# Kernel optimization log

Hardware: AMD Instinct MI355X
Metric: run time of the kernel (lower is better)

## Reference

```python
import jax, jax.numpy as jnp
import numpy as np

QMAX = 7.0      # symmetric int4 magnitude
GROUP = 64      # weight quant group size along input dim
RANK = 32       # SVD low-rank correction rank
EPS = 1e-8


def quantize_act(x):
    # per-token symmetric int4 fake-quant: scale = max|x| / 7 over feature dim
    s = jnp.maximum(jnp.max(jnp.abs(x), axis=-1, keepdims=True) / QMAX, EPS)
    q = jnp.clip(jnp.round(x / s), -8.0, 7.0)
    return q * s


def quantize_weight(w):
    # per-output-channel, per-group (GROUP along input dim) symmetric int4 fake-quant
    O, D = w.shape
    wg = w.reshape(O, D // GROUP, GROUP)
    s = jnp.maximum(jnp.max(jnp.abs(wg), axis=-1, keepdims=True) / QMAX, EPS)
    q = jnp.clip(jnp.round(wg / s), -8.0, 7.0)
    return (q * s).reshape(O, D)


def setup_inputs() -> dict:
    key = jax.random.key(0)
    k0, k1, k2, k3 = jax.random.split(key, 4)
    dim_in, dim_out2 = 3072, 24576
    x = jax.random.normal(k0, (1, 4096, dim_in), dtype=jnp.float32)
    w_res = jax.random.normal(k1, (dim_out2, dim_in), dtype=jnp.float32) * 0.02
    lora_down = jax.random.normal(k2, (RANK, dim_in), dtype=jnp.float32) * 0.02
    lora_up = jax.random.normal(k3, (dim_out2, RANK), dtype=jnp.float32) * 0.02
    return {"x": x, "w_res": w_res, "lora_down": lora_down, "lora_up": lora_up}


def reference(x, w_res, lora_down, lora_up):
    # SVDQW4A4Linear: quantized residual matmul + fp low-rank correction
    xq = quantize_act(x)                        # [B, S, D]
    wq = quantize_weight(w_res)                 # [O, D]
    out = jnp.einsum('bsd,od->bso', xq, wq)
    out = out + jnp.einsum('bsr,or->bso', jnp.einsum('bsd,rd->bsr', x, lora_down), lora_up)
    # GEGLU epilogue: chunk(2, dim=-1), x * gelu(gate)  (torch F.gelu = exact erf)
    h, gate = jnp.split(out, 2, axis=-1)
    return h * jax.nn.gelu(gate, approximate=False)
```

## Files before the change

### kernel.cpp

```cpp
#include <hip/hip_runtime.h>
#include <hip/hip_bf16.h>
#include <math.h>

typedef __bf16 bf16_t;
typedef __bf16 bf16x4 __attribute__((ext_vector_type(4)));
typedef __bf16 bf16x8 __attribute__((ext_vector_type(8)));
typedef float  f32x4  __attribute__((ext_vector_type(4)));

#define DIN   3072
#define NOUT  24576
#define HALF  12288
#define MTOK  4096
#define BM    128
#define BN    128
#define BK    64

#define GLD16(gp, lp) \
    __builtin_amdgcn_global_load_lds((const __attribute__((address_space(1))) void*)(gp), \
                                     (__attribute__((address_space(3))) void*)(lp), 16, 0, 0)

__global__ __launch_bounds__(256) void k_quant_x(const float* __restrict__ x,
                                                 bf16_t* __restrict__ xq) {
    int m = blockIdx.x;
    int t = threadIdx.x;
    const float4* row = reinterpret_cast<const float4*>(x + (size_t)m * DIN);
    float4 v[3];
    float vm = 0.f;
#pragma unroll
    for (int i = 0; i < 3; ++i) {
        v[i] = row[t + i * 256];
        vm = fmaxf(vm, fmaxf(fmaxf(fabsf(v[i].x), fabsf(v[i].y)),
                             fmaxf(fabsf(v[i].z), fabsf(v[i].w))));
    }
#pragma unroll
    for (int d = 1; d < 64; d <<= 1) vm = fmaxf(vm, __shfl_xor(vm, d));
    __shared__ float sm[4];
    if ((t & 63) == 0) sm[t >> 6] = vm;
    __syncthreads();
    vm = fmaxf(fmaxf(sm[0], sm[1]), fmaxf(sm[2], sm[3]));
    float s = fmaxf(vm * (1.f / 7.f), 1e-8f);
    float inv = 1.f / s;
    bf16x4* orow = reinterpret_cast<bf16x4*>(xq + (size_t)m * DIN);
#pragma unroll
    for (int i = 0; i < 3; ++i) {
        bf16x4 o;
        o[0] = (bf16_t)(fminf(fmaxf(rintf(v[i].x * inv), -8.f), 7.f) * s);
        o[1] = (bf16_t)(fminf(fmaxf(rintf(v[i].y * inv), -8.f), 7.f) * s);
        o[2] = (bf16_t)(fminf(fmaxf(rintf(v[i].z * inv), -8.f), 7.f) * s);
        o[3] = (bf16_t)(fminf(fmaxf(rintf(v[i].w * inv), -8.f), 7.f) * s);
        orow[t + i * 256] = o;
    }
}

__global__ __launch_bounds__(256) void k_quant_w(const float* __restrict__ w,
                                                 bf16_t* __restrict__ wq) {
    size_t idx = (size_t)blockIdx.x * 256 + threadIdx.x;
    float4 v = reinterpret_cast<const float4*>(w)[idx];
    float vm = fmaxf(fmaxf(fabsf(v.x), fabsf(v.y)), fmaxf(fabsf(v.z), fabsf(v.w)));
    vm = fmaxf(vm, __shfl_xor(vm, 1));
    vm = fmaxf(vm, __shfl_xor(vm, 2));
    vm = fmaxf(vm, __shfl_xor(vm, 4));
    vm = fmaxf(vm, __shfl_xor(vm, 8));
    float s = fmaxf(vm * (1.f / 7.f), 1e-8f);
    float inv = 1.f / s;
    bf16x4 o;
    o[0] = (bf16_t)(fminf(fmaxf(rintf(v.x * inv), -8.f), 7.f) * s);
    o[1] = (bf16_t)(fminf(fmaxf(rintf(v.y * inv), -8.f), 7.f) * s);
    o[2] = (bf16_t)(fminf(fmaxf(rintf(v.z * inv), -8.f), 7.f) * s);
    o[3] = (bf16_t)(fminf(fmaxf(rintf(v.w * inv), -8.f), 7.f) * s);
    reinterpret_cast<bf16x4*>(wq)[idx] = o;
}

__global__ __launch_bounds__(256) void k_lora_t(const float* __restrict__ x,
                                                const float* __restrict__ ld,
                                                bf16_t* __restrict__ T) {
    int r = threadIdx.x & 31;
    int m = blockIdx.x * 8 + (threadIdx.x >> 5);
    const float4* xr = reinterpret_cast<const float4*>(x + (size_t)m * DIN);
    const float4* lr = reinterpret_cast<const float4*>(ld + (size_t)r * DIN);
    float acc = 0.f;
#pragma unroll 4
    for (int i = 0; i < DIN / 4; ++i) {
        float4 a = xr[i], b = lr[i];
        acc += a.x * b.x + a.y * b.y + a.z * b.z + a.w * b.w;
    }
    T[(size_t)m * 32 + r] = (bf16_t)acc;
}

__global__ __launch_bounds__(256) void k_cvt_lu(const float* __restrict__ lu,
                                                bf16_t* __restrict__ lub) {
    size_t idx = (size_t)blockIdx.x * 256 + threadIdx.x;
    float4 v = reinterpret_cast<const float4*>(lu)[idx];
    bf16x4 o;
    o[0] = (bf16_t)v.x; o[1] = (bf16_t)v.y; o[2] = (bf16_t)v.z; o[3] = (bf16_t)v.w;
    reinterpret_cast<bf16x4*>(lub)[idx] = o;
}

__global__ __launch_bounds__(512, 2) void k_gemm(const bf16_t* __restrict__ xq,
                                                 const bf16_t* __restrict__ wq,
                                                 const bf16_t* __restrict__ T,
                                                 const bf16_t* __restrict__ lub,
                                                 float* __restrict__ out) {
    __shared__ __align__(16) char smem[65536];
    bf16_t* sA = (bf16_t*)smem;
    bf16_t* sH = sA + BM * BK;
    bf16_t* sG = sH + BN * BK;

    int tid = threadIdx.x, lane = tid & 63, w = tid >> 6;
    int half = w >> 2;
    int wr = (w & 3) >> 1, wc = w & 1;

    int nwg = gridDim.x;
    int cpx = nwg >> 3;
    int swz = (blockIdx.x & 7) * cpx + (blockIdx.x >> 3);
    int mt = swz & 31, nt = swz >> 5;
    int m0 = mt * BM, c0 = nt * BN;

    f32x4 acc[4][4];
#pragma unroll
    for (int i = 0; i < 4; ++i)
#pragma unroll
        for (int j = 0; j < 4; ++j) acc[i][j] = (f32x4){0.f, 0.f, 0.f, 0.f};

    const bf16_t* bsrc = wq + (size_t)(c0 + half * HALF) * DIN;
    const char* sBb = (const char*)(half ? sG : sH);
    const char* sAb = (const char*)sA;

    for (int k0 = 0; k0 < DIN; k0 += BK) {
        __syncthreads();
#pragma unroll
        for (int r = 0; r < 2; ++r) {
            int chunk = r * 512 + tid;
            int row = chunk >> 3;
            int gc = ((chunk & 7) ^ (row & 7)) * 8;
            int ldsoff = r * 4096 + w * 512;
            GLD16(xq + (size_t)(m0 + row) * DIN + k0 + gc, sA + ldsoff);
            GLD16(wq + (size_t)(c0 + row) * DIN + k0 + gc, sH + ldsoff);
            GLD16(wq + (size_t)(c0 + HALF + row) * DIN + k0 + gc, sG + ldsoff);
        }
        __syncthreads();

#pragma unroll
        for (int ks = 0; ks < 2; ++ks) {
            int c16 = ks * 4 + (lane >> 4);
            bf16x8 a[4], b[4];
#pragma unroll
            for (int i = 0; i < 4; ++i) {
                int ra = wr * 64 + i * 16 + (lane & 15);
                int rb = wc * 64 + i * 16 + (lane & 15);
                a[i] = *reinterpret_cast<const bf16x8*>(sAb + ra * 128 + ((c16 ^ (ra & 7)) << 4));
                b[i] = *reinterpret_cast<const bf16x8*>(sBb + rb * 128 + ((c16 ^ (rb & 7)) << 4));
            }
#pragma unroll
            for (int m = 0; m < 4; ++m)
#pragma unroll
                for (int n = 0; n < 4; ++n)
                    acc[m][n] = __builtin_amdgcn_mfma_f32_16x16x32_bf16(a[m], b[n], acc[m][n], 0, 0, 0);
        }
    }

    {
        bf16x8 tf[4];
#pragma unroll
        for (int m = 0; m < 4; ++m)
            tf[m] = *reinterpret_cast<const bf16x8*>(
                T + (size_t)(m0 + wr * 64 + m * 16 + (lane & 15)) * 32 + (lane >> 4) * 8);
#pragma unroll
        for (int n = 0; n < 4; ++n) {
            bf16x8 lu = *reinterpret_cast<const bf16x8*>(
                lub + (size_t)(c0 + half * HALF + wc * 64 + n * 16 + (lane & 15)) * 32 + (lane >> 4) * 8);
#pragma unroll
            for (int m = 0; m < 4; ++m)
                acc[m][n] = __builtin_amdgcn_mfma_f32_16x16x32_bf16(tf[m], lu, acc[m][n], 0, 0, 0);
        }
    }

    __syncthreads();
    float* exch = (float*)smem;
    if (half) {
#pragma unroll
        for (int m = 0; m < 4; ++m)
#pragma unroll
            for (int n = 0; n < 4; ++n) {
                int col = wc * 64 + n * 16 + (lane & 15);
#pragma unroll
                for (int r = 0; r < 4; ++r) {
                    int row = wr * 64 + m * 16 + (lane >> 4) * 4 + r;
                    float g = acc[m][n][r];
                    float gl = 0.5f * g * (1.0f + erff(g * 0.70710678118654752f));
                    exch[row * 128 + (col ^ (((row >> 2) & 3) << 4))] = gl;
                }
            }
    }
    __syncthreads();
    if (!half) {
#pragma unroll
        for (int m = 0; m < 4; ++m)
#pragma unroll
            for (int n = 0; n < 4; ++n) {
                int col = wc * 64 + n * 16 + (lane & 15);
#pragma unroll
                for (int r = 0; r < 4; ++r) {
                    int row = wr * 64 + m * 16 + (lane >> 4) * 4 + r;
                    float gl = exch[row * 128 + (col ^ (((row >> 2) & 3) << 4))];
                    out[(size_t)(m0 + row) * HALF + c0 + col] = acc[m][n][r] * gl;
                }
            }
    }
}

extern "C" void kernel_launch(void* const* d_in, const int* in_sizes, int n_in,
                              void* d_out, int out_size, void* d_ws, size_t ws_size,
                              hipStream_t stream) {
    const float* x  = (const float*)d_in[0];
    const float* wr = (const float*)d_in[1];
    const float* ld = (const float*)d_in[2];
    const float* lu = (const float*)d_in[3];
    float* out = (float*)d_out;

    bf16_t* xq  = (bf16_t*)d_ws;
    bf16_t* wq  = xq + (size_t)MTOK * DIN;
    bf16_t* T   = wq + (size_t)NOUT * DIN;
    bf16_t* lub = T  + (size_t)MTOK * 32;

    k_quant_x<<<MTOK, 256, 0, stream>>>(x, xq);
    k_quant_w<<<(NOUT * (DIN / 4)) / 256, 256, 0, stream>>>(wr, wq);
    k_lora_t<<<MTOK / 8, 256, 0, stream>>>(x, ld, T);
    k_cvt_lu<<<(NOUT * 32 / 4) / 256, 256, 0, stream>>>(lu, lub);
    k_gemm<<<(MTOK / BM) * (HALF / BN), 512, 0, stream>>>(xq, wq, T, lub, out);
}
```

Before: 922.7 us.

## Double-buffer GEMM with 256-row tiles and interleaved async loads and MFMA phases

```diff
diff --git a/kernel.cpp b/kernel.cpp
--- a/kernel.cpp
+++ b/kernel.cpp
@@ -11,13 +11,18 @@
 #define NOUT  24576
 #define HALF  12288
 #define MTOK  4096
-#define BM    128
-#define BN    128
 #define BK    64
+#define NT    48
 
 #define GLD16(gp, lp) \
     __builtin_amdgcn_global_load_lds((const __attribute__((address_space(1))) void*)(gp), \
                                      (__attribute__((address_space(3))) void*)(lp), 16, 0, 0)
+
+#define BAR()    __builtin_amdgcn_s_barrier()
+#define LGKM0()  asm volatile("s_waitcnt lgkmcnt(0)" ::: "memory")
+#define WAITV(N) asm volatile("s_waitcnt vmcnt(" #N ")" ::: "memory")
+#define PRIO1()  __builtin_amdgcn_s_setprio(1)
+#define PRIO0()  __builtin_amdgcn_s_setprio(0)
 
 __global__ __launch_bounds__(256) void k_quant_x(const float* __restrict__ x,
                                                  bf16_t* __restrict__ xq) {
@@ -96,96 +101,143 @@
     reinterpret_cast<bf16x4*>(lub)[idx] = o;
 }
 
+
+#define STAGE_UNIT(gbase, sbase)                                              \
+    do {                                                                      \
+        _Pragma("unroll")                                                     \
+        for (int _r = 0; _r < 2; ++_r) {                                      \
+            int _c = _r * 512 + tid;                                          \
+            int _row = _c >> 3;                                               \
+            int _gc = ((_c & 7) ^ (_row & 7)) * 8;                            \
+            GLD16((gbase) + (size_t)_row * DIN + _gc, (sbase) + _c * 16);     \
+        }                                                                     \
+    } while (0)
+
+#define LOAD_A(mh)                                                            \
+    _Pragma("unroll")                                                         \
+    for (int _i = 0; _i < 4; ++_i) {                                          \
+        _Pragma("unroll")                                                     \
+        for (int _ks = 0; _ks < 2; ++_ks) {                                   \
+            int _ra = (mh) * 128 + wr * 64 + _i * 16 + l15;                   \
+            int _c16 = _ks * 4 + lhi;                                         \
+            a[_i][_ks] = *(const bf16x8*)(sAc + _ra * 128 + ((_c16 ^ lk) << 4)); \
+        }                                                                     \
+    }
+
+#define LOAD_B(nh)                                                            \
+    _Pragma("unroll")                                                         \
+    for (int _j = 0; _j < 2; ++_j) {                                          \
+        _Pragma("unroll")                                                     \
+        for (int _ks = 0; _ks < 2; ++_ks) {                                   \
+            int _rb = wc * 64 + ((nh) * 2 + _j) * 16 + l15;                   \
+            int _c16 = _ks * 4 + lhi;                                         \
+            b[(nh) * 2 + _j][_ks] = *(const bf16x8*)(sBc + _rb * 128 + ((_c16 ^ lk) << 4)); \
+        }                                                                     \
+    }
+
+#define MFMA_Q(mh, nh)                                                        \
+    _Pragma("unroll")                                                         \
+    for (int _i = 0; _i < 4; ++_i) {                                          \
+        _Pragma("unroll")                                                     \
+        for (int _j = 0; _j < 2; ++_j) {                                      \
+            _Pragma("unroll")                                                 \
+            for (int _ks = 0; _ks < 2; ++_ks) {                               \
+                acc[(mh) * 4 + _i][(nh) * 2 + _j] =                           \
+                    __builtin_amdgcn_mfma_f32_16x16x32_bf16(                  \
+                        a[_i][_ks], b[(nh) * 2 + _j][_ks],                    \
+                        acc[(mh) * 4 + _i][(nh) * 2 + _j], 0, 0, 0);          \
+            }                                                                 \
+        }                                                                     \
+    }
+
 __global__ __launch_bounds__(512, 2) void k_gemm(const bf16_t* __restrict__ xq,
                                                  const bf16_t* __restrict__ wq,
                                                  const bf16_t* __restrict__ T,
                                                  const bf16_t* __restrict__ lub,
                                                  float* __restrict__ out) {
-    __shared__ __align__(16) char smem[65536];
-    bf16_t* sA = (bf16_t*)smem;
-    bf16_t* sH = sA + BM * BK;
-    bf16_t* sG = sH + BN * BK;
-
-    int tid = threadIdx.x, lane = tid & 63, w = tid >> 6;
-    int half = w >> 2;
-    int wr = (w & 3) >> 1, wc = w & 1;
-
-    int nwg = gridDim.x;
-    int cpx = nwg >> 3;
-    int swz = (blockIdx.x & 7) * cpx + (blockIdx.x >> 3);
-    int mt = swz & 31, nt = swz >> 5;
-    int m0 = mt * BM, c0 = nt * BN;
-
-    f32x4 acc[4][4];
-#pragma unroll
-    for (int i = 0; i < 4; ++i)
+    __shared__ __align__(16) char smem[131072];
+
+    const int tid = threadIdx.x, lane = tid & 63, w = tid >> 6;
+    const int half = w >> 2;
+    const int wr = (w >> 1) & 1, wc = w & 1;
+    const int l15 = lane & 15, lhi = lane >> 4, lk = lane & 7;
+
+    const int nwg = gridDim.x;
+    const int cpx = nwg >> 3;
+    const int swz = ((int)blockIdx.x & 7) * cpx + ((int)blockIdx.x >> 3);
+    const int mt = swz & 15, nt = swz >> 4;
+    const int m0 = mt * 256, c0 = nt * 128;
+
+    f32x4 acc[8][4];
+#pragma unroll
+    for (int i = 0; i < 8; ++i)
 #pragma unroll
         for (int j = 0; j < 4; ++j) acc[i][j] = (f32x4){0.f, 0.f, 0.f, 0.f};
 
-    const bf16_t* bsrc = wq + (size_t)(c0 + half * HALF) * DIN;
-    const char* sBb = (const char*)(half ? sG : sH);
-    const char* sAb = (const char*)sA;
-
-    for (int k0 = 0; k0 < DIN; k0 += BK) {
-        __syncthreads();
-#pragma unroll
-        for (int r = 0; r < 2; ++r) {
-            int chunk = r * 512 + tid;
-            int row = chunk >> 3;
-            int gc = ((chunk & 7) ^ (row & 7)) * 8;
-            int ldsoff = r * 4096 + w * 512;
-            GLD16(xq + (size_t)(m0 + row) * DIN + k0 + gc, sA + ldsoff);
-            GLD16(wq + (size_t)(c0 + row) * DIN + k0 + gc, sH + ldsoff);
-            GLD16(wq + (size_t)(c0 + HALF + row) * DIN + k0 + gc, sG + ldsoff);
+    const bf16_t* gA = xq + (size_t)m0 * DIN;
+    const bf16_t* gH = wq + (size_t)c0 * DIN;
+    const bf16_t* gG = wq + (size_t)(c0 + HALF) * DIN;
+
+    STAGE_UNIT(gA, smem);
+    STAGE_UNIT(gH, smem + 32768);
+    STAGE_UNIT(gG, smem + 49152);
+    STAGE_UNIT(gA + (size_t)128 * DIN, smem + 16384);
+    WAITV(2);
+    BAR();
+
+    int cur = 0;
+    for (int t = 0; t < NT; ++t) {
+        const int kc = (t + 1 < NT) ? (t + 1) * BK : t * BK;
+        char* sw = smem + (cur ^ 1) * 65536;
+        const char* sAc = smem + cur * 65536;
+        const char* sBc = sAc + 32768 + half * 16384;
+
+        bf16x8 a[4][2], b[4][2];
+
+        LOAD_A(0); LOAD_B(0);
+        STAGE_UNIT(gA + kc, sw);
+        BAR(); LGKM0(); PRIO1(); MFMA_Q(0, 0); PRIO0(); BAR();
+        LOAD_B(1);
+        STAGE_UNIT(gH + kc, sw + 32768);
+        BAR(); LGKM0(); PRIO1(); MFMA_Q(0, 1); PRIO0(); WAITV(4); BAR();
+        LOAD_A(1);
+        STAGE_UNIT(gG + kc, sw + 49152);
+        BAR(); LGKM0(); PRIO1(); MFMA_Q(1, 0); PRIO0(); BAR();
+        STAGE_UNIT(gA + (size_t)128 * DIN + kc, sw + 16384);
+        BAR(); LGKM0(); PRIO1(); MFMA_Q(1, 1); PRIO0(); WAITV(2); BAR();
+
+        cur ^= 1;
+    }
+
+    {
+        bf16x8 tf[8];
+#pragma unroll
+        for (int m = 0; m < 8; ++m) {
+            int row = m0 + (m >> 2) * 128 + wr * 64 + (m & 3) * 16 + l15;
+            tf[m] = *reinterpret_cast<const bf16x8*>(T + (size_t)row * 32 + lhi * 8);
         }
-        __syncthreads();
-
-#pragma unroll
-        for (int ks = 0; ks < 2; ++ks) {
-            int c16 = ks * 4 + (lane >> 4);
-            bf16x8 a[4], b[4];
-#pragma unroll
-            for (int i = 0; i < 4; ++i) {
-                int ra = wr * 64 + i * 16 + (lane & 15);
-                int rb = wc * 64 + i * 16 + (lane & 15);
-                a[i] = *reinterpret_cast<const bf16x8*>(sAb + ra * 128 + ((c16 ^ (ra & 7)) << 4));
-                b[i] = *reinterpret_cast<const bf16x8*>(sBb + rb * 128 + ((c16 ^ (rb & 7)) << 4));
-            }
-#pragma unroll
-            for (int m = 0; m < 4; ++m)
-#pragma unroll
-                for (int n = 0; n < 4; ++n)
-                    acc[m][n] = __builtin_amdgcn_mfma_f32_16x16x32_bf16(a[m], b[n], acc[m][n], 0, 0, 0);
-        }
-    }
-
-    {
-        bf16x8 tf[4];
-#pragma unroll
-        for (int m = 0; m < 4; ++m)
-            tf[m] = *reinterpret_cast<const bf16x8*>(
-                T + (size_t)(m0 + wr * 64 + m * 16 + (lane & 15)) * 32 + (lane >> 4) * 8);
 #pragma unroll
         for (int n = 0; n < 4; ++n) {
-            bf16x8 lu = *reinterpret_cast<const bf16x8*>(
-                lub + (size_t)(c0 + half * HALF + wc * 64 + n * 16 + (lane & 15)) * 32 + (lane >> 4) * 8);
-#pragma unroll
-            for (int m = 0; m < 4; ++m)
+            int ocol = c0 + half * HALF + wc * 64 + n * 16 + l15;
+            bf16x8 lu = *reinterpret_cast<const bf16x8*>(lub + (size_t)ocol * 32 + lhi * 8);
+#pragma unroll
+            for (int m = 0; m < 8; ++m)
                 acc[m][n] = __builtin_amdgcn_mfma_f32_16x16x32_bf16(tf[m], lu, acc[m][n], 0, 0, 0);
         }
     }
 
+    WAITV(0);
     __syncthreads();
     float* exch = (float*)smem;
     if (half) {
 #pragma unroll
-        for (int m = 0; m < 4; ++m)
+        for (int m = 0; m < 8; ++m)
 #pragma unroll
             for (int n = 0; n < 4; ++n) {
-                int col = wc * 64 + n * 16 + (lane & 15);
+                int col = wc * 64 + n * 16 + l15;
 #pragma unroll
                 for (int r = 0; r < 4; ++r) {
-                    int row = wr * 64 + m * 16 + (lane >> 4) * 4 + r;
+                    int row = (m >> 2) * 128 + wr * 64 + (m & 3) * 16 + lhi * 4 + r;
                     float g = acc[m][n][r];
                     float gl = 0.5f * g * (1.0f + erff(g * 0.70710678118654752f));
                     exch[row * 128 + (col ^ (((row >> 2) & 3) << 4))] = gl;
@@ -195,13 +247,13 @@
     __syncthreads();
     if (!half) {
 #pragma unroll
-        for (int m = 0; m < 4; ++m)
+        for (int m = 0; m < 8; ++m)
 #pragma unroll
             for (int n = 0; n < 4; ++n) {
-                int col = wc * 64 + n * 16 + (lane & 15);
+                int col = wc * 64 + n * 16 + l15;
 #pragma unroll
                 for (int r = 0; r < 4; ++r) {
-                    int row = wr * 64 + m * 16 + (lane >> 4) * 4 + r;
+                    int row = (m >> 2) * 128 + wr * 64 + (m & 3) * 16 + lhi * 4 + r;
                     float gl = exch[row * 128 + (col ^ (((row >> 2) & 3) << 4))];
                     out[(size_t)(m0 + row) * HALF + c0 + col] = acc[m][n][r] * gl;
                 }
@@ -227,5 +279,5 @@
     k_quant_w<<<(NOUT * (DIN / 4)) / 256, 256, 0, stream>>>(wr, wq);
     k_lora_t<<<MTOK / 8, 256, 0, stream>>>(x, ld, T);
     k_cvt_lu<<<(NOUT * 32 / 4) / 256, 256, 0, stream>>>(lu, lub);
-    k_gemm<<<(MTOK / BM) * (HALF / BN), 512, 0, stream>>>(xq, wq, T, lub, out);
-}
+    k_gemm<<<(MTOK / 256) * (HALF / 128), 512, 0, stream>>>(xq, wq, T, lub, out);
+}
```

Result: faster. 891.0 us (-3.4%).
